# Performance work log

Measured on AMD Instinct MI355X. Metric: run time of the kernel, lower is better.

Reference implementation:

```python
import jax, jax.numpy as jnp
import numpy as np

D_MODEL = 1024
B, N = 8, 2048

def setup_inputs() -> dict:
    key = jax.random.key(0)
    k1, k2, k3 = jax.random.split(key, 3)
    x = jax.random.normal(k1, (B, N, D_MODEL), dtype=jnp.float32)
    W_qkv = jax.random.normal(k2, (3 * D_MODEL, D_MODEL), dtype=jnp.float32) * (D_MODEL ** -0.5)
    b_qkv = jax.random.normal(k3, (3 * D_MODEL,), dtype=jnp.float32) * 0.02
    return {"x": x, "W_qkv": W_qkv, "b_qkv": b_qkv}

def reference(x, W_qkv, b_qkv):
    d = x.shape[-1]
    scale = d ** 0.5
    # qkv projection: torch Linear computes x @ W.T + b
    qkv = jnp.einsum('bnc,oc->bno', x, W_qkv) + b_qkv  # [B, N, 3d]
    q, k, v = jnp.split(qkv, 3, axis=-1)               # each [B, N, d]
    scores = jnp.einsum('bqd,bkd->bqk', q, k) / scale  # [B, N, N]
    attn = jax.nn.softmax(scores, axis=-1)
    return jnp.einsum('bqk,bkd->bqd', attn, v)         # [B, N, d]
```

## Files before the change

### kernel.cpp

```cpp
#include <hip/hip_runtime.h>


#define AS1 __attribute__((address_space(1)))
#define AS3 __attribute__((address_space(3)))

typedef __bf16 bfrag  __attribute__((ext_vector_type(8)));
typedef float  ffrag  __attribute__((ext_vector_type(4)));
typedef __bf16 bf16x4 __attribute__((ext_vector_type(4)));
typedef __bf16 bf16x8 __attribute__((ext_vector_type(8)));

__global__ __launch_bounds__(256) void cvt_f32_bf16(const float* __restrict__ in,
                                                    __bf16* __restrict__ out, int n4) {
  int i = blockIdx.x * blockDim.x + threadIdx.x;
  int stride = gridDim.x * blockDim.x;
  for (; i < n4; i += stride) {
    float4 v = ((const float4*)in)[i];
    bf16x4 o;
    o[0] = (__bf16)v.x; o[1] = (__bf16)v.y; o[2] = (__bf16)v.z; o[3] = (__bf16)v.w;
    ((bf16x4*)out)[i] = o;
  }
}

__device__ __forceinline__ void stage_half(
    const __bf16* __restrict__ Atile, const __bf16* __restrict__ Btile,
    int lda, int ldb, int nT, __bf16* lds, int tid, int t, int h) {
  const int te = (t < nT) ? t : (t - 2);
  const int kt = te * 64;
  const __bf16* src = (h < 2) ? Atile : Btile;
  const int ld = (h < 2) ? lda : ldb;
  const int row0 = (h & 1) * 128;
  __bf16* dst = lds + (te & 1) * 32768 + h * 8192;
#pragma unroll
  for (int l = 0; l < 2; ++l) {
    const int y = l * 4096 + tid * 8;
    const int r = y >> 6;
    const int c = ((tid & 7) * 8) ^ ((r & 7) << 3);
    __builtin_amdgcn_global_load_lds((AS1 void*)(src + (size_t)(row0 + r) * ld + kt + c),
                                     (AS3 void*)(dst + y), 16, 0, 0);
  }
}

__device__ __forceinline__ void rd_b(const __bf16* lds, int bufoff, int bRowBase,
                                     int ck0, int ck1, bfrag b[4][2]) {
#pragma unroll
  for (int j = 0; j < 4; ++j) {
    const int off = bufoff + bRowBase + (j >> 1) * 8192 + (j & 1) * 1024;
    b[j][0] = *(const bfrag*)&lds[off + ck0];
    b[j][1] = *(const bfrag*)&lds[off + ck1];
  }
}

template <int QA>
__device__ __forceinline__ void rd_a(const __bf16* lds, int bufoff, int aRowBase,
                                     int ck0, int ck1, bfrag a[4][2]) {
#pragma unroll
  for (int m = 0; m < 4; ++m) {
    const int off = bufoff + aRowBase + QA * 8192 + m * 1024;
    a[m][0] = *(const bfrag*)&lds[off + ck0];
    a[m][1] = *(const bfrag*)&lds[off + ck1];
  }
}

template <int QA>
__device__ __forceinline__ void mfma_q(const bfrag a[4][2], const bfrag b[4][2],
                                       ffrag acc[8][4]) {
#pragma unroll
  for (int m = 0; m < 4; ++m)
#pragma unroll
    for (int j = 0; j < 4; ++j)
#pragma unroll
      for (int ks = 0; ks < 2; ++ks)
        acc[QA * 4 + m][j] = __builtin_amdgcn_mfma_f32_16x16x32_bf16(
            a[m][ks], b[j][ks], acc[QA * 4 + m][j], 0, 0, 0);
}

#define SYNC_MFMA(QA)                                                          \
    asm volatile("s_waitcnt vmcnt(8)" ::: "memory");                           \
    __builtin_amdgcn_sched_barrier(0);                                         \
    __builtin_amdgcn_s_barrier();                                              \
    __builtin_amdgcn_s_setprio(1);                                             \
    mfma_q<QA>(a, b, acc);                                                     \
    __builtin_amdgcn_s_setprio(0);                                             \
    __builtin_amdgcn_s_barrier();                                              \
    __builtin_amdgcn_sched_barrier(0);

#define STG(T, H) stage_half(Atile, Btile, lda, ldb, nT, lds, tid, (T), (H))

__device__ __forceinline__ void gemm256_mainloop(
    const __bf16* __restrict__ Atile, const __bf16* __restrict__ Btile,
    int lda, int ldb, int K, __bf16* lds, ffrag acc[8][4]) {
  const int tid  = threadIdx.x;
  const int lane = tid & 63;
  const int wid  = tid >> 6;
  const int wr   = wid >> 2, wc = wid & 3;
  const int fr   = lane & 15;
  const int fk   = (lane >> 4) * 8;
  const int swz  = (fr & 7) << 3;
  const int ck0  = fk ^ swz;
  const int ck1  = (32 + fk) ^ swz;
  const int aRowBase = (wr * 64 + fr) * 64;
  const int bRowBase = 16384 + (wc * 32 + fr) * 64;
  const int nT = K >> 6;

  STG(0, 2); STG(0, 3); STG(0, 0); STG(0, 1);
  STG(1, 2); STG(1, 3); STG(1, 0);
  asm volatile("s_waitcnt vmcnt(8)" ::: "memory");
  __builtin_amdgcn_s_barrier();
  __builtin_amdgcn_sched_barrier(0);

  const int nIter = nT >> 1;
#pragma unroll 1
  for (int i = 0; i < nIter; ++i) {
    const int t1 = 2 * i + 1, t2 = 2 * i + 2, t3 = 2 * i + 3;
    bfrag a[4][2], b[4][2];
    rd_b(lds, 0, bRowBase, ck0, ck1, b);
    rd_a<0>(lds, 0, aRowBase, ck0, ck1, a);
    STG(t1, 1);
    SYNC_MFMA(0)
    rd_a<1>(lds, 0, aRowBase, ck0, ck1, a);
    STG(t2, 2); STG(t2, 3); STG(t2, 0);
    SYNC_MFMA(1)
    rd_b(lds, 32768, bRowBase, ck0, ck1, b);
    rd_a<0>(lds, 32768, aRowBase, ck0, ck1, a);
    STG(t2, 1);
    SYNC_MFMA(0)
    rd_a<1>(lds, 32768, aRowBase, ck0, ck1, a);
    STG(t3, 2); STG(t3, 3); STG(t3, 0);
    SYNC_MFMA(1)
  }
}

#define ACC_ZERO()                                                             \
  ffrag acc[8][4];                                                             \
  _Pragma("unroll") for (int m = 0; m < 8; ++m)                                \
  _Pragma("unroll") for (int n = 0; n < 4; ++n) acc[m][n] = (ffrag)(0.0f);


__global__ __launch_bounds__(512, 2) void qkv_gemm256(
    const __bf16* __restrict__ Abf, const __bf16* __restrict__ Wbf,
    const float* __restrict__ bias,
    __bf16* __restrict__ Q, __bf16* __restrict__ Ko, __bf16* __restrict__ Vt) {
  __shared__ __bf16 lds[65536];
  ACC_ZERO();
  int bid = (int)blockIdx.x;
  bid = (bid & 7) * 96 + (bid >> 3);
  const int brow = (bid / 12) * 256;
  const int bcol = (bid % 12) * 256;
  gemm256_mainloop(Abf + (size_t)brow * 1024, Wbf + (size_t)bcol * 1024,
                   1024, 1024, 1024, lds, acc);
  const int lane = threadIdx.x & 63, wid = threadIdx.x >> 6;
  const int wr = wid >> 2, wc = wid & 3;
  const int region = bcol >> 10;
  if (region < 2) {
    __bf16* dst = region == 0 ? Q : Ko;
    const float scale = region == 0 ? 0.03125f : 1.0f;
#pragma unroll
    for (int j = 0; j < 4; ++j) {
      const int qb = j >> 1, n = j & 1;
      const int col = bcol + qb * 128 + wc * 32 + n * 16 + (lane & 15);
      const int o = col & 1023;
      const float bv = bias[col];
#pragma unroll
      for (int i = 0; i < 8; ++i) {
        const int qa = i >> 2, m = i & 3;
#pragma unroll
        for (int r = 0; r < 4; ++r) {
          const int mg = brow + qa * 128 + wr * 64 + m * 16 + (lane >> 4) * 4 + r;
          dst[(size_t)mg * 1024 + o] = (__bf16)((acc[i][j][r] + bv) * scale);
        }
      }
    }
  } else {
#pragma unroll
    for (int j = 0; j < 4; ++j) {
      const int qb = j >> 1, n = j & 1;
      const int col = bcol + qb * 128 + wc * 32 + n * 16 + (lane & 15);
      const int o = col & 1023;
      const float bv = bias[col];
#pragma unroll
      for (int i = 0; i < 8; ++i) {
        const int qa = i >> 2, m = i & 3;
        const int mg0 = brow + qa * 128 + wr * 64 + m * 16 + (lane >> 4) * 4;
        const int b = mg0 >> 11, nr = mg0 & 2047;
        bf16x4 v;
#pragma unroll
        for (int r = 0; r < 4; ++r) v[r] = (__bf16)(acc[i][j][r] + bv);
        *(bf16x4*)&Vt[(size_t)b * 2097152 + (size_t)o * 2048 + nr] = v;
      }
    }
  }
}

__global__ __launch_bounds__(512, 2) void scores_gemm256(const __bf16* __restrict__ Q,
                                                         const __bf16* __restrict__ Kb,
                                                         __bf16* __restrict__ S) {
  __shared__ __bf16 lds[65536];
  ACC_ZERO();
  int bid = (int)blockIdx.x;
  const int wg = (bid & 7) * 64 + (bid >> 3);
  const int brow = (wg & 7) * 256, bcol = ((wg >> 3) & 7) * 256, z = wg >> 6;
  gemm256_mainloop(Q + (size_t)z * 2048 * 1024 + (size_t)brow * 1024,
                   Kb + (size_t)z * 2048 * 1024 + (size_t)bcol * 1024,
                   1024, 1024, 1024, lds, acc);
  const int lane = threadIdx.x & 63, wid = threadIdx.x >> 6;
  const int wr = wid >> 2, wc = wid & 3;
#pragma unroll
  for (int j = 0; j < 4; ++j) {
    const int qb = j >> 1, n = j & 1;
    const int o = bcol + qb * 128 + wc * 32 + n * 16 + (lane & 15);
#pragma unroll
    for (int i = 0; i < 8; ++i) {
      const int qa = i >> 2, m = i & 3;
#pragma unroll
      for (int r = 0; r < 4; ++r) {
        const int mg = brow + qa * 128 + wr * 64 + m * 16 + (lane >> 4) * 4 + r;
        S[((size_t)(z * 2048 + mg)) * 2048 + o] = (__bf16)acc[i][j][r];
      }
    }
  }
}

__global__ __launch_bounds__(256) void softmax_bf16(__bf16* S) {
  const int row = blockIdx.x * 4 + (threadIdx.x >> 6);
  const int lane = threadIdx.x & 63;
  __bf16* s = S + (size_t)row * 2048 + lane * 8;
  float f[32];
#pragma unroll
  for (int c = 0; c < 4; ++c) {
    bf16x8 v = *(const bf16x8*)&s[c * 512];
#pragma unroll
    for (int j = 0; j < 8; ++j) f[c * 8 + j] = (float)v[j];
  }
  float m = f[0];
#pragma unroll
  for (int j = 1; j < 32; ++j) m = fmaxf(m, f[j]);
#pragma unroll
  for (int off = 32; off; off >>= 1) m = fmaxf(m, __shfl_xor(m, off, 64));
  float sum = 0.f;
#pragma unroll
  for (int j = 0; j < 32; ++j) { f[j] = __expf(f[j] - m); sum += f[j]; }
#pragma unroll
  for (int off = 32; off; off >>= 1) sum += __shfl_xor(sum, off, 64);
  const float inv = 1.0f / sum;
#pragma unroll
  for (int c = 0; c < 4; ++c) {
    bf16x8 o;
#pragma unroll
    for (int j = 0; j < 8; ++j) o[j] = (__bf16)(f[c * 8 + j] * inv);
    *(bf16x8*)&s[c * 512] = o;
  }
}

__global__ __launch_bounds__(512, 2) void pv_gemm256(const __bf16* __restrict__ P,
                                                     const __bf16* __restrict__ Vt,
                                                     float* __restrict__ O) {
  __shared__ __bf16 lds[65536];
  ACC_ZERO();
  int bid = (int)blockIdx.x;
  const int wg = (bid & 7) * 32 + (bid >> 3);
  const int brow = (wg & 7) * 256, bcol = ((wg >> 3) & 3) * 256, z = wg >> 5;
  gemm256_mainloop(P + (size_t)(z * 2048 + brow) * 2048,
                   Vt + (size_t)z * 1024 * 2048 + (size_t)bcol * 2048,
                   2048, 2048, 2048, lds, acc);
  const int lane = threadIdx.x & 63, wid = threadIdx.x >> 6;
  const int wr = wid >> 2, wc = wid & 3;
#pragma unroll
  for (int j = 0; j < 4; ++j) {
    const int qb = j >> 1, n = j & 1;
    const int o = bcol + qb * 128 + wc * 32 + n * 16 + (lane & 15);
#pragma unroll
    for (int i = 0; i < 8; ++i) {
      const int qa = i >> 2, m = i & 3;
#pragma unroll
      for (int r = 0; r < 4; ++r) {
        const int mg = brow + qa * 128 + wr * 64 + m * 16 + (lane >> 4) * 4 + r;
        O[((size_t)(z * 2048 + mg)) * 1024 + o] = acc[i][j][r];
      }
    }
  }
}

extern "C" void kernel_launch(void* const* d_in, const int* in_sizes, int n_in,
                              void* d_out, int out_size, void* d_ws, size_t ws_size,
                              hipStream_t stream) {
  (void)in_sizes; (void)n_in; (void)out_size; (void)ws_size;
  const float* x    = (const float*)d_in[0];
  const float* W    = (const float*)d_in[1];
  const float* bias = (const float*)d_in[2];
  float* out = (float*)d_out;
  char* ws = (char*)d_ws;
  const size_t MB = 1u << 20;
  __bf16* x_bf = (__bf16*)(ws + 0);
  __bf16* W_bf = (__bf16*)(ws + 32 * MB);
  __bf16* Qb   = (__bf16*)(ws + 38 * MB);
  __bf16* Kb   = (__bf16*)(ws + 70 * MB);
  __bf16* S    = (__bf16*)(ws + 102 * MB);
  __bf16* Vt   = (__bf16*)(ws + 166 * MB);

  cvt_f32_bf16<<<2048, 256, 0, stream>>>(x, x_bf, 16777216 / 4);
  cvt_f32_bf16<<<1024, 256, 0, stream>>>(W, W_bf, 3145728 / 4);
  qkv_gemm256<<<768, 512, 0, stream>>>(x_bf, W_bf, bias, Qb, Kb, Vt);
  scores_gemm256<<<512, 512, 0, stream>>>(Qb, Kb, S);
  softmax_bf16<<<4096, 256, 0, stream>>>(S);
  pv_gemm256<<<256, 512, 0, stream>>>(S, Vt, out);
}
```

Before: 285.8 us.

## Split GEMM mainloop into eight quadrant phases with interleaved staging

The 256-tile GEMM mainloop now runs eight smaller MFMA phases per iteration instead of four. Each phase covers an A-half by B-half quadrant and uses separate B fragment registers for each half. Global-to-LDS staging loads are spread one per phase, with the vmcnt wait moved to every fourth phase and an explicit lgkmcnt wait added. This aims to overlap LDS reads and global loads with compute more finely and to cut the B fragment register footprint. In exchange it doubles the number of block barriers per iteration.

After: 278.4 us. 2.6% less time.

```diff
diff --git a/kernel.cpp b/kernel.cpp
--- a/kernel.cpp
+++ b/kernel.cpp
@@ -21,10 +21,10 @@
   }
 }
 
+
 __device__ __forceinline__ void stage_half(
     const __bf16* __restrict__ Atile, const __bf16* __restrict__ Btile,
-    int lda, int ldb, int nT, __bf16* lds, int tid, int t, int h) {
-  const int te = (t < nT) ? t : (t - 2);
+    int lda, int ldb, __bf16* lds, int tid, int te, int h) {
   const int kt = te * 64;
   const __bf16* src = (h < 2) ? Atile : Btile;
   const int ld = (h < 2) ? lda : ldb;
@@ -40,16 +40,6 @@
   }
 }
 
-__device__ __forceinline__ void rd_b(const __bf16* lds, int bufoff, int bRowBase,
-                                     int ck0, int ck1, bfrag b[4][2]) {
-#pragma unroll
-  for (int j = 0; j < 4; ++j) {
-    const int off = bufoff + bRowBase + (j >> 1) * 8192 + (j & 1) * 1024;
-    b[j][0] = *(const bfrag*)&lds[off + ck0];
-    b[j][1] = *(const bfrag*)&lds[off + ck1];
-  }
-}
-
 template <int QA>
 __device__ __forceinline__ void rd_a(const __bf16* lds, int bufoff, int aRowBase,
                                      int ck0, int ck1, bfrag a[4][2]) {
@@ -61,30 +51,36 @@
   }
 }
 
-template <int QA>
-__device__ __forceinline__ void mfma_q(const bfrag a[4][2], const bfrag b[4][2],
-                                       ffrag acc[8][4]) {
-#pragma unroll
-  for (int m = 0; m < 4; ++m)
-#pragma unroll
-    for (int j = 0; j < 4; ++j)
-#pragma unroll
-      for (int ks = 0; ks < 2; ++ks)
-        acc[QA * 4 + m][j] = __builtin_amdgcn_mfma_f32_16x16x32_bf16(
-            a[m][ks], b[j][ks], acc[QA * 4 + m][j], 0, 0, 0);
-}
-
-#define SYNC_MFMA(QA)                                                          \
-    asm volatile("s_waitcnt vmcnt(8)" ::: "memory");                           \
-    __builtin_amdgcn_sched_barrier(0);                                         \
+template <int QB>
+__device__ __forceinline__ void rd_bq(const __bf16* lds, int bufoff, int bRowBase,
+                                      int ck0, int ck1, bfrag b[2][2]) {
+#pragma unroll
+  for (int n = 0; n < 2; ++n) {
+    const int off = bufoff + bRowBase + QB * 8192 + n * 1024;
+    b[n][0] = *(const bfrag*)&lds[off + ck0];
+    b[n][1] = *(const bfrag*)&lds[off + ck1];
+  }
+}
+
+#define PH(QA, QB, BREG, DOVM)                                                 \
+  {                                                                            \
+    if (DOVM) asm volatile("s_waitcnt vmcnt(6)" ::: "memory");                 \
     __builtin_amdgcn_s_barrier();                                              \
+    asm volatile("s_waitcnt lgkmcnt(0)" ::: "memory");                         \
     __builtin_amdgcn_s_setprio(1);                                             \
-    mfma_q<QA>(a, b, acc);                                                     \
+    _Pragma("unroll") for (int m_ = 0; m_ < 4; ++m_)                           \
+    _Pragma("unroll") for (int n_ = 0; n_ < 2; ++n_)                           \
+    _Pragma("unroll") for (int ks_ = 0; ks_ < 2; ++ks_)                        \
+      acc[(QA) * 4 + m_][(QB) * 2 + n_] =                                      \
+          __builtin_amdgcn_mfma_f32_16x16x32_bf16(                             \
+              a[m_][ks_], BREG[n_][ks_], acc[(QA) * 4 + m_][(QB) * 2 + n_],    \
+              0, 0, 0);                                                        \
     __builtin_amdgcn_s_setprio(0);                                             \
     __builtin_amdgcn_s_barrier();                                              \
-    __builtin_amdgcn_sched_barrier(0);
-
-#define STG(T, H) stage_half(Atile, Btile, lda, ldb, nT, lds, tid, (T), (H))
+    __builtin_amdgcn_sched_barrier(0);                                         \
+  }
+
+#define STG(TE, H) stage_half(Atile, Btile, lda, ldb, lds, tid, (TE), (H))
 
 __device__ __forceinline__ void gemm256_mainloop(
     const __bf16* __restrict__ Atile, const __bf16* __restrict__ Btile,
@@ -102,31 +98,42 @@
   const int bRowBase = 16384 + (wc * 32 + fr) * 64;
   const int nT = K >> 6;
 
-  STG(0, 2); STG(0, 3); STG(0, 0); STG(0, 1);
-  STG(1, 2); STG(1, 3); STG(1, 0);
-  asm volatile("s_waitcnt vmcnt(8)" ::: "memory");
+  STG(0, 0); STG(0, 2); STG(0, 3); STG(0, 1);
+  STG(1, 0); STG(1, 2); STG(1, 3);
+  asm volatile("s_waitcnt vmcnt(6)" ::: "memory");
   __builtin_amdgcn_s_barrier();
-  __builtin_amdgcn_sched_barrier(0);
 
   const int nIter = nT >> 1;
 #pragma unroll 1
   for (int i = 0; i < nIter; ++i) {
-    const int t1 = 2 * i + 1, t2 = 2 * i + 2, t3 = 2 * i + 3;
-    bfrag a[4][2], b[4][2];
-    rd_b(lds, 0, bRowBase, ck0, ck1, b);
+    const int t1  = 2 * i + 1;
+    const int t2e = (2 * i + 2 < nT) ? (2 * i + 2) : (2 * i);
+    const int t3e = (2 * i + 3 < nT) ? (2 * i + 3) : (2 * i + 1);
+    bfrag a[4][2], b0f[2][2], b1f[2][2];
     rd_a<0>(lds, 0, aRowBase, ck0, ck1, a);
+    rd_bq<0>(lds, 0, bRowBase, ck0, ck1, b0f);
     STG(t1, 1);
-    SYNC_MFMA(0)
+    PH(0, 0, b0f, false)
+    rd_bq<1>(lds, 0, bRowBase, ck0, ck1, b1f);
+    STG(t2e, 0);
+    PH(0, 1, b1f, false)
     rd_a<1>(lds, 0, aRowBase, ck0, ck1, a);
-    STG(t2, 2); STG(t2, 3); STG(t2, 0);
-    SYNC_MFMA(1)
-    rd_b(lds, 32768, bRowBase, ck0, ck1, b);
+    STG(t2e, 2);
+    PH(1, 1, b1f, false)
+    STG(t2e, 3);
+    PH(1, 0, b0f, true)
     rd_a<0>(lds, 32768, aRowBase, ck0, ck1, a);
-    STG(t2, 1);
-    SYNC_MFMA(0)
+    rd_bq<0>(lds, 32768, bRowBase, ck0, ck1, b0f);
+    STG(t2e, 1);
+    PH(0, 0, b0f, false)
+    rd_bq<1>(lds, 32768, bRowBase, ck0, ck1, b1f);
+    STG(t3e, 0);
+    PH(0, 1, b1f, false)
     rd_a<1>(lds, 32768, aRowBase, ck0, ck1, a);
-    STG(t3, 2); STG(t3, 3); STG(t3, 0);
-    SYNC_MFMA(1)
+    STG(t3e, 2);
+    PH(1, 1, b1f, false)
+    STG(t3e, 3);
+    PH(1, 0, b0f, true)
   }
 }
 
```
